# Optimization experiments

Measured on AMD Instinct MI355X. Metric: run time of the kernel, lower is better.

## Reference

```python
import jax, jax.numpy as jnp
import numpy as np

EMBED_DIM = 768
NUM_HEADS = 12
HEAD_DIM = EMBED_DIM // NUM_HEADS
SCALE = HEAD_DIM ** -0.5
LN_EPS = 1e-5


def layer_norm(x, gamma, beta):
    mu = jnp.mean(x, axis=-1, keepdims=True)
    var = jnp.var(x, axis=-1, keepdims=True)
    return (x - mu) * jax.lax.rsqrt(var + LN_EPS) * gamma + beta


def setup_inputs() -> dict:
    key = jax.random.key(0)
    ks = jax.random.split(key, 10)
    B, N, M, C = 4, 4096, 256, EMBED_DIM
    inp = {
        "input_tokens": jax.random.normal(ks[0], (B, N, C), dtype=jnp.float32),
        "query_tokens": jax.random.normal(ks[1], (B, M, C), dtype=jnp.float32),
        "Wq": jax.random.normal(ks[2], (C, C), dtype=jnp.float32) * 0.02,
        "bq": jnp.zeros((C,), dtype=jnp.float32),
        "Wk": jax.random.normal(ks[3], (C, C), dtype=jnp.float32) * 0.02,
        "bk": jnp.zeros((C,), dtype=jnp.float32),
        "Wv": jax.random.normal(ks[4], (C, C), dtype=jnp.float32) * 0.02,
        "bv": jnp.zeros((C,), dtype=jnp.float32),
        "gq_ln": jnp.ones((C,), dtype=jnp.float32),
        "bq_ln": jnp.zeros((C,), dtype=jnp.float32),
        "gk_ln": jnp.ones((C,), dtype=jnp.float32),
        "bk_ln": jnp.zeros((C,), dtype=jnp.float32),
    }
    return inp


def reference(input_tokens, query_tokens, Wq, bq, Wk, bk, Wv, bv,
              gq_ln, bq_ln, gk_ln, bk_ln):
    B, N, C = input_tokens.shape
    _, M, _ = query_tokens.shape
    H, D = NUM_HEADS, HEAD_DIM

    # v: Linear only (no LayerNorm on the attn=None path)
    v = (input_tokens @ Wv.T + bv).reshape(B, N, H, D).transpose(0, 2, 1, 3)   # [B,H,N,D]
    # q, k: Linear -> LayerNorm over full embed_dim, then split heads
    q = layer_norm(query_tokens @ Wq.T + bq, gq_ln, bq_ln)
    q = q.reshape(B, M, H, D).transpose(0, 2, 1, 3) * SCALE                    # [B,H,M,D]
    k = layer_norm(input_tokens @ Wk.T + bk, gk_ln, bk_ln)
    k = k.reshape(B, N, H, D).transpose(0, 2, 1, 3)                            # [B,H,N,D]

    attn = jax.nn.softmax(jnp.einsum('bhmd,bhnd->bhmn', q, k), axis=-1)        # [B,H,M,N]
    out = jnp.einsum('bhmn,bhnd->bhmd', attn, v)                               # [B,H,M,D]
    out = out.transpose(0, 2, 1, 3).reshape(B, M, C)
    return (query_tokens + out, attn)
```

## Files before the change

### kernel.cpp

```cpp
#include <hip/hip_runtime.h>
#include <math.h>

#define BB 4
#define NN 4096
#define MM 256
#define CC 768
#define HH 12
#define DD 64
#define SCALEF 0.125f
#define LN_EPSF 1e-5f

typedef __attribute__((ext_vector_type(4))) float f32x4;
typedef __attribute__((ext_vector_type(16))) float f32x16;
typedef __attribute__((ext_vector_type(8))) _Float16 f16x8;
typedef __attribute__((ext_vector_type(4))) _Float16 f16x4;

__device__ __forceinline__ void gldh(const _Float16* g, _Float16* l) {
    __builtin_amdgcn_global_load_lds(
        (const __attribute__((address_space(1))) void*)g,
        (__attribute__((address_space(3))) void*)l, 16, 0, 0);
}

__global__ __launch_bounds__(256) void conv_f16(
    const float* __restrict__ x, _Float16* __restrict__ y, long long n)
{
    long long i = ((long long)blockIdx.x * 256 + threadIdx.x) * 8;
    const long long stride = (long long)gridDim.x * 256 * 8;
    for (; i < n; i += stride) {
        float4 a = *(const float4*)(x + i);
        float4 b = *(const float4*)(x + i + 4);
        f16x8 o;
        o[0] = (_Float16)a.x; o[1] = (_Float16)a.y;
        o[2] = (_Float16)a.z; o[3] = (_Float16)a.w;
        o[4] = (_Float16)b.x; o[5] = (_Float16)b.y;
        o[6] = (_Float16)b.z; o[7] = (_Float16)b.w;
        *(f16x8*)(y + i) = o;
    }
}

__global__ __launch_bounds__(256) void proj_gemm_f16(
    const _Float16* __restrict__ Xh,
    const _Float16* __restrict__ X2h,
    const _Float16* __restrict__ Wkh, const _Float16* __restrict__ Wqh,
    const _Float16* __restrict__ Wvh,
    const float* __restrict__ bk, const float* __restrict__ bq,
    const float* __restrict__ bv,
    _Float16* __restrict__ Klin, _Float16* __restrict__ Qlin,
    _Float16* __restrict__ Vth)
{
    __shared__ _Float16 As[2][128 * 32];
    __shared__ _Float16 Bs[2][128 * 32];

    const int bid = blockIdx.x;
    const _Float16* Ag; const _Float16* Bg;
    const float* bias; _Float16* out = nullptr;
    int sid, bm, bn;
    bool isV = false;
    if (bid < 768) {
        sid = bid; Ag = Xh; Bg = Wkh; bias = bk; out = Klin;
        bm = sid & 127; bn = sid >> 7;
    } else if (bid < 816) {
        sid = bid - 768; Ag = X2h; Bg = Wqh; bias = bq; out = Qlin;
        bm = sid & 7; bn = sid >> 3;
    } else {
        sid = bid - 816; Ag = Xh; Bg = Wvh; bias = bv; isV = true;
        bm = sid & 127; bn = sid >> 7;
    }
    const int row0 = bm * 128, col0 = bn * 128;

    const int tid = threadIdx.x;
    const int w = tid >> 6, lane = tid & 63;
    const int wr = w >> 1, wc = w & 1;
    const int fr = lane & 15, kg = lane >> 4;

    f32x4 acc[4][4];
#pragma unroll
    for (int m = 0; m < 4; ++m)
#pragma unroll
        for (int n = 0; n < 4; ++n)
            acc[m][n] = (f32x4){0.f, 0.f, 0.f, 0.f};

#define STAGE(sel, kt)                                                          \
    do {                                                                        \
        const int kk = (kt) << 5;                                               \
        _Pragma("unroll")                                                       \
        for (int i = 0; i < 2; ++i) {                                           \
            const int cbase = (i * 4 + w) * 64;                                 \
            const int c = cbase + lane;                                         \
            const int row = c >> 2, ks = (c & 3) << 3;                          \
            gldh(Ag + (size_t)(row0 + row) * CC + kk + ks, &As[sel][cbase * 8]);\
            gldh(Bg + (size_t)(col0 + row) * CC + kk + ks, &Bs[sel][cbase * 8]);\
        }                                                                       \
    } while (0)

    STAGE(0, 0);
    int cur = 0;
    const int nk = CC >> 5;
    for (int kt = 0; kt < nk; ++kt) {
        __syncthreads();
        if (kt + 1 < nk) STAGE(cur ^ 1, kt + 1);
        const _Float16* lA = As[cur];
        const _Float16* lB = Bs[cur];
        f16x8 a[4], b[4];
#pragma unroll
        for (int m = 0; m < 4; ++m)
            a[m] = *(const f16x8*)(lA + (wr * 64 + m * 16 + fr) * 32 + kg * 8);
#pragma unroll
        for (int n = 0; n < 4; ++n)
            b[n] = *(const f16x8*)(lB + (wc * 64 + n * 16 + fr) * 32 + kg * 8);
        __builtin_amdgcn_s_setprio(1);
#pragma unroll
        for (int m = 0; m < 4; ++m)
#pragma unroll
            for (int n = 0; n < 4; ++n)
                acc[m][n] = __builtin_amdgcn_mfma_f32_16x16x32_f16(
                    a[m], b[n], acc[m][n], 0, 0, 0);
        __builtin_amdgcn_s_setprio(0);
        cur ^= 1;
    }
#undef STAGE

    if (!isV) {
        float bvv[4];
#pragma unroll
        for (int n = 0; n < 4; ++n)
            bvv[n] = bias[col0 + wc * 64 + n * 16 + fr];
#pragma unroll
        for (int m = 0; m < 4; ++m)
#pragma unroll
            for (int n = 0; n < 4; ++n) {
                const int col = col0 + wc * 64 + n * 16 + fr;
#pragma unroll
                for (int r = 0; r < 4; ++r) {
                    const int row = row0 + wr * 64 + m * 16 + kg * 4 + r;
                    out[(size_t)row * CC + col] = (_Float16)(acc[m][n][r] + bvv[n]);
                }
            }
    } else {
        const int b = row0 >> 12;
        const int rb = row0 & 4095;
#pragma unroll
        for (int n = 0; n < 4; ++n) {
            const int cg = col0 + wc * 64 + n * 16 + fr;
            const int hh = cg >> 6, d = cg & 63;
            const float bb = bias[cg];
            _Float16* vrow = Vth + ((size_t)((b * HH + hh) * DD + d)) * NN + rb + wr * 64;
#pragma unroll
            for (int m = 0; m < 4; ++m) {
                f16x4 v4;
#pragma unroll
                for (int r = 0; r < 4; ++r)
                    v4[r] = (_Float16)(acc[m][n][r] + bb);
                *(f16x4*)(vrow + m * 16 + kg * 4) = v4;
            }
        }
    }
}

__global__ __launch_bounds__(256) void ln_rows_f16(
    const _Float16* __restrict__ Y, _Float16* __restrict__ outh,
    const float* __restrict__ g, const float* __restrict__ be, const float scale)
{
    const int row = blockIdx.x;
    const _Float16* y = Y + (size_t)row * CC;
    const int tid = threadIdx.x;
    float x0 = (float)y[tid], x1 = (float)y[tid + 256], x2 = (float)y[tid + 512];
    float s = x0 + x1 + x2;
    float q = x0 * x0 + x1 * x1 + x2 * x2;
#pragma unroll
    for (int o = 32; o >= 1; o >>= 1) {
        s += __shfl_xor(s, o, 64);
        q += __shfl_xor(q, o, 64);
    }
    __shared__ float sh_s[4], sh_q[4];
    const int w = tid >> 6;
    if ((tid & 63) == 0) { sh_s[w] = s; sh_q[w] = q; }
    __syncthreads();
    s = sh_s[0] + sh_s[1] + sh_s[2] + sh_s[3];
    q = sh_q[0] + sh_q[1] + sh_q[2] + sh_q[3];
    const float mu  = s * (1.f / 768.f);
    const float var = q * (1.f / 768.f) - mu * mu;
    const float inv = rsqrtf(var + LN_EPSF);
    _Float16* o = outh + (size_t)row * CC;
    o[tid]       = (_Float16)(((x0 - mu) * inv * g[tid]       + be[tid])       * scale);
    o[tid + 256] = (_Float16)(((x1 - mu) * inv * g[tid + 256] + be[tid + 256]) * scale);
    o[tid + 512] = (_Float16)(((x2 - mu) * inv * g[tid + 512] + be[tid + 512]) * scale);
}

__global__ __launch_bounds__(256, 2) void fused_attn(
    const _Float16* __restrict__ Qh,
    const _Float16* __restrict__ Kh,
    const _Float16* __restrict__ Vt,
    const float* __restrict__ qtok,
    float* __restrict__ attn, float* __restrict__ out0)
{
    __shared__ __align__(16) unsigned char smem[78848];
    _Float16* Kl = (_Float16*)smem;
    _Float16* Vl = (_Float16*)(smem + 32768);
    _Float16* Ql = (_Float16*)(smem + 65536);
    _Float16* Pl = (_Float16*)(smem + 69632);
    float (*red)[32][2] = (float(*)[32][2])(smem + 77824);
    float* rbuf = (float*)smem;

    const int tid = threadIdx.x;
    const int w = tid >> 6, lane = tid & 63;
    const int l5 = lane >> 5, lm = lane & 31;
    const int bh = blockIdx.x % 48;
    const int mt = blockIdx.x / 48;
    const int h = bh % HH, b = bh / HH;
    const int qr0 = mt * 32;

#define STAGEK(sel, c0)                                                         \
    _Pragma("unroll")                                                           \
    for (int i = 0; i < 4; ++i) {                                               \
        const int L = i * 256 + tid;                                            \
        const int n = L >> 3, pos = L & 7;                                      \
        gldh(Kh + (size_t)(b * NN + (c0) + n) * CC + h * DD + ((pos ^ (n & 7)) << 3), \
             &Kl[(sel) * 8192 + (i * 256 + w * 64) * 8]);                       \
    }
#define STAGEV(sel, c0)                                                         \
    _Pragma("unroll")                                                           \
    for (int i = 0; i < 4; ++i) {                                               \
        const int L = i * 256 + tid;                                            \
        const int d = L >> 4, pos = L & 15;                                     \
        const int blk = (pos & 8) | ((pos & 7) ^ (d & 7));                      \
        gldh(Vt + (size_t)(bh * DD + d) * NN + (c0) + blk * 8,                  \
             &Vl[(sel) * 8192 + (i * 256 + w * 64) * 8]);                       \
    }

    {
        const int n = tid >> 3, pos = tid & 7;
        gldh(Qh + (size_t)(b * MM + qr0 + n) * CC + h * DD + ((pos ^ (n & 7)) << 3),
             &Ql[(w * 64) * 8]);
    }
    STAGEK(0, 0);
    __syncthreads();
    f16x8 qf[4];
#pragma unroll
    for (int ks = 0; ks < 4; ++ks)
        qf[ks] = *(const f16x8*)&Ql[lm * 64 + (((ks * 2 + l5) ^ (lm & 7)) << 3)];

    const int nl = w * 32 + lm;

    float mrun = -1e30f, srun = 0.f;
    int cur = 0;
    for (int c = 0; c < 32; ++c) {
        if (c) __syncthreads();
        if (c + 1 < 32) STAGEK(cur ^ 1, (c + 1) * 128);
        const _Float16* Kb = Kl + cur * 8192;
        f32x16 s;
#pragma unroll
        for (int r = 0; r < 16; ++r) s[r] = 0.f;
        __builtin_amdgcn_s_setprio(1);
#pragma unroll
        for (int ks = 0; ks < 4; ++ks) {
            f16x8 kf = *(const f16x8*)&Kb[nl * 64 + (((ks * 2 + l5) ^ (nl & 7)) << 3)];
            s = __builtin_amdgcn_mfma_f32_32x32x16_f16(kf, qf[ks], s, 0, 0, 0);
        }
        __builtin_amdgcn_s_setprio(0);
        float cmax = s[0];
#pragma unroll
        for (int r = 1; r < 16; ++r) cmax = fmaxf(cmax, s[r]);
        cmax = fmaxf(cmax, __shfl_xor(cmax, 32, 64));
        const float nm = fmaxf(mrun, cmax);
        float cs = 0.f;
#pragma unroll
        for (int r = 0; r < 16; ++r) cs += __expf(s[r] - nm);
        cs += __shfl_xor(cs, 32, 64);
        srun = srun * __expf(mrun - nm) + cs;
        mrun = nm;
        cur ^= 1;
    }
    if (lane < 32) { red[w][lane][0] = mrun; red[w][lane][1] = srun; }
    __syncthreads();
    float M = -1e30f;
#pragma unroll
    for (int ww = 0; ww < 4; ++ww) M = fmaxf(M, red[ww][lm][0]);
    float S = 0.f;
#pragma unroll
    for (int ww = 0; ww < 4; ++ww) S += red[ww][lm][1] * __expf(red[ww][lm][0] - M);
    const float invS = 1.f / S;

    f32x16 oacc[2];
#pragma unroll
    for (int dt = 0; dt < 2; ++dt)
#pragma unroll
        for (int r = 0; r < 16; ++r) oacc[dt][r] = 0.f;

    float* attnRow = attn + ((size_t)(bh * MM + qr0 + lm)) * NN;

    STAGEK(0, 0); STAGEV(0, 0);
    cur = 0;
    for (int c = 0; c < 32; ++c) {
        __syncthreads();
        if (c + 1 < 32) { STAGEK(cur ^ 1, (c + 1) * 128); STAGEV(cur ^ 1, (c + 1) * 128); }
        const _Float16* Kb = Kl + cur * 8192;
        const _Float16* Vb = Vl + cur * 8192;
        f32x16 s;
#pragma unroll
        for (int r = 0; r < 16; ++r) s[r] = 0.f;
        __builtin_amdgcn_s_setprio(1);
#pragma unroll
        for (int ks = 0; ks < 4; ++ks) {
            f16x8 kf = *(const f16x8*)&Kb[nl * 64 + (((ks * 2 + l5) ^ (nl & 7)) << 3)];
            s = __builtin_amdgcn_mfma_f32_32x32x16_f16(kf, qf[ks], s, 0, 0, 0);
        }
        __builtin_amdgcn_s_setprio(0);
#pragma unroll
        for (int q = 0; q < 4; ++q) {
            float4 pw;
            f16x4 ph;
#pragma unroll
            for (int r = 0; r < 4; ++r) {
                const float p = __expf(s[q * 4 + r] - M) * invS;
                ((float*)&pw)[r] = p;
                ph[r] = (_Float16)p;
            }
            *(float4*)(attnRow + c * 128 + w * 32 + q * 8 + l5 * 4) = pw;
            const int blk16 = w * 4 + q;
            const int pos = (blk16 & 8) | ((blk16 & 7) ^ (lm & 7));
            *(f16x4*)&Pl[lm * 128 + pos * 8 + l5 * 4] = ph;
        }
        __builtin_amdgcn_s_setprio(1);
#pragma unroll
        for (int ks = 0; ks < 2; ++ks) {
            const int blk16 = w * 4 + ks * 2 + l5;
            const int posP = (blk16 & 8) | ((blk16 & 7) ^ (lm & 7));
            f16x8 pf = *(const f16x8*)&Pl[lm * 128 + posP * 8];
#pragma unroll
            for (int dt = 0; dt < 2; ++dt) {
                const int d = dt * 32 + lm;
                const int posV = (blk16 & 8) | ((blk16 & 7) ^ (d & 7));
                f16x8 vf = *(const f16x8*)&Vb[d * 128 + posV * 8];
                oacc[dt] = __builtin_amdgcn_mfma_f32_32x32x16_f16(pf, vf, oacc[dt], 0, 0, 0);
            }
        }
        __builtin_amdgcn_s_setprio(0);
        cur ^= 1;
    }

    __syncthreads();
#pragma unroll
    for (int dt = 0; dt < 2; ++dt)
#pragma unroll
        for (int r = 0; r < 16; ++r) {
            const int mrow = (r & 3) + 8 * (r >> 2) + 4 * l5;
            rbuf[w * 2048 + mrow * 64 + dt * 32 + lm] = oacc[dt][r];
        }
    __syncthreads();
    {
        const int m = tid >> 3, d0 = (tid & 7) * 8;
        const size_t obase = (size_t)(b * MM + qr0 + m) * CC + h * DD + d0;
#pragma unroll
        for (int j = 0; j < 8; ++j) {
            const int idx = m * 64 + d0 + j;
            float v = rbuf[idx] + rbuf[2048 + idx] + rbuf[4096 + idx] + rbuf[6144 + idx];
            out0[obase + j] = v + qtok[obase + j];
        }
    }
#undef STAGEK
#undef STAGEV
}

extern "C" void kernel_launch(void* const* d_in, const int* in_sizes, int n_in,
                              void* d_out, int out_size, void* d_ws, size_t ws_size,
                              hipStream_t stream) {
    (void)in_sizes; (void)n_in; (void)out_size; (void)ws_size;
    const float* input_tokens = (const float*)d_in[0];
    const float* query_tokens = (const float*)d_in[1];
    const float* Wq   = (const float*)d_in[2];
    const float* bq   = (const float*)d_in[3];
    const float* Wk   = (const float*)d_in[4];
    const float* bk   = (const float*)d_in[5];
    const float* Wv   = (const float*)d_in[6];
    const float* bv   = (const float*)d_in[7];
    const float* gq   = (const float*)d_in[8];
    const float* bqln = (const float*)d_in[9];
    const float* gk   = (const float*)d_in[10];
    const float* bkln = (const float*)d_in[11];

    float* out0 = (float*)d_out;
    float* attn = out0 + (size_t)BB * MM * CC;

    _Float16* h   = (_Float16*)d_ws;
    _Float16* Klin = h;
    _Float16* Qlin = Klin + (size_t)BB * NN * CC;
    _Float16* Xh   = Qlin + (size_t)BB * MM * CC;
    _Float16* X2h  = Xh   + (size_t)BB * NN * CC;
    _Float16* Wkh  = X2h  + (size_t)BB * MM * CC;
    _Float16* Wqh  = Wkh  + (size_t)CC * CC;
    _Float16* Wvh  = Wqh  + (size_t)CC * CC;
    _Float16* Kh   = Wvh  + (size_t)CC * CC;
    _Float16* Qh   = Kh   + (size_t)BB * NN * CC;
    _Float16* Vt   = Qh   + (size_t)BB * MM * CC;

    conv_f16<<<2048, 256, 0, stream>>>(input_tokens, Xh, (long long)BB * NN * CC);
    conv_f16<<<384, 256, 0, stream>>>(query_tokens, X2h, (long long)BB * MM * CC);
    conv_f16<<<288, 256, 0, stream>>>(Wk, Wkh, (long long)CC * CC);
    conv_f16<<<288, 256, 0, stream>>>(Wq, Wqh, (long long)CC * CC);
    conv_f16<<<288, 256, 0, stream>>>(Wv, Wvh, (long long)CC * CC);

    proj_gemm_f16<<<1584, 256, 0, stream>>>(Xh, X2h, Wkh, Wqh, Wvh,
                                            bk, bq, bv, Klin, Qlin, Vt);

    ln_rows_f16<<<BB * NN, 256, 0, stream>>>(Klin, Kh, gk, bkln, 1.0f);
    ln_rows_f16<<<BB * MM, 256, 0, stream>>>(Qlin, Qh, gq, bqln, SCALEF);

    fused_attn<<<BB * HH * (MM / 32), 256, 0, stream>>>(Qh, Kh, Vt, query_tokens,
                                                        attn, out0);
}
```

Before: 215.4 us.

## Split attention over key dimension into stats, main and reduce kernels

The single fused attention kernel, which launched only 384 blocks, becomes three kernels that split the key sequence into four chunks for 1536 blocks. A stats kernel computes per-chunk row max and sum, the main kernel merges them, writes normalized attention probabilities and partial P·V outputs, and a reduce kernel sums the partials and adds the query residual. The aim is to fill the MI355X compute units, which were under-occupied. The cost is two extra launches and extra global traffic for the stats and partial buffers.

```diff
diff --git a/kernel.cpp b/kernel.cpp
--- a/kernel.cpp
+++ b/kernel.cpp
@@ -187,28 +187,117 @@
     o[tid + 512] = (_Float16)(((x2 - mu) * inv * g[tid + 512] + be[tid + 512]) * scale);
 }
 
-__global__ __launch_bounds__(256, 2) void fused_attn(
+__global__ __launch_bounds__(256, 4) void attn_stats(
     const _Float16* __restrict__ Qh,
     const _Float16* __restrict__ Kh,
+    float* __restrict__ stats)
+{
+    __shared__ __align__(16) unsigned char smem[37888];
+    _Float16* Kl = (_Float16*)smem;
+    _Float16* Ql = (_Float16*)(smem + 32768);
+    float (*red)[32][2] = (float(*)[32][2])(smem + 36864);
+
+    const int tid = threadIdx.x;
+    const int w = tid >> 6, lane = tid & 63;
+    const int l5 = lane >> 5, lm = lane & 31;
+    const int bid = blockIdx.x;
+    const int mt = bid / 192;
+    const int rem = bid % 192;
+    const int bh = rem >> 2, ns = rem & 3;
+    const int h = bh % HH, b = bh / HH;
+    const int qr0 = mt * 32;
+    const int nb = ns * 1024;
+
+#define STAGEK(sel, c0)                                                         \
+    _Pragma("unroll")                                                           \
+    for (int i = 0; i < 4; ++i) {                                               \
+        const int L = i * 256 + tid;                                            \
+        const int n = L >> 3, pos = L & 7;                                      \
+        gldh(Kh + (size_t)(b * NN + (c0) + n) * CC + h * DD + ((pos ^ (n & 7)) << 3), \
+             &Kl[(sel) * 8192 + (i * 256 + w * 64) * 8]);                       \
+    }
+
+    {
+        const int n = tid >> 3, pos = tid & 7;
+        gldh(Qh + (size_t)(b * MM + qr0 + n) * CC + h * DD + ((pos ^ (n & 7)) << 3),
+             &Ql[(w * 64) * 8]);
+    }
+    STAGEK(0, nb);
+    __syncthreads();
+    f16x8 qf[4];
+#pragma unroll
+    for (int ks = 0; ks < 4; ++ks)
+        qf[ks] = *(const f16x8*)&Ql[lm * 64 + (((ks * 2 + l5) ^ (lm & 7)) << 3)];
+
+    const int nl = w * 32 + lm;
+
+    float mrun = -1e30f, srun = 0.f;
+    int cur = 0;
+    for (int c = 0; c < 8; ++c) {
+        if (c) __syncthreads();
+        if (c + 1 < 8) STAGEK(cur ^ 1, nb + (c + 1) * 128);
+        const _Float16* Kb = Kl + cur * 8192;
+        f32x16 s;
+#pragma unroll
+        for (int r = 0; r < 16; ++r) s[r] = 0.f;
+        __builtin_amdgcn_s_setprio(1);
+#pragma unroll
+        for (int ks = 0; ks < 4; ++ks) {
+            f16x8 kf = *(const f16x8*)&Kb[nl * 64 + (((ks * 2 + l5) ^ (nl & 7)) << 3)];
+            s = __builtin_amdgcn_mfma_f32_32x32x16_f16(kf, qf[ks], s, 0, 0, 0);
+        }
+        __builtin_amdgcn_s_setprio(0);
+        float cmax = s[0];
+#pragma unroll
+        for (int r = 1; r < 16; ++r) cmax = fmaxf(cmax, s[r]);
+        cmax = fmaxf(cmax, __shfl_xor(cmax, 32, 64));
+        const float nm = fmaxf(mrun, cmax);
+        float cs = 0.f;
+#pragma unroll
+        for (int r = 0; r < 16; ++r) cs += __expf(s[r] - nm);
+        cs += __shfl_xor(cs, 32, 64);
+        srun = srun * __expf(mrun - nm) + cs;
+        mrun = nm;
+        cur ^= 1;
+    }
+    if (lane < 32) { red[w][lane][0] = mrun; red[w][lane][1] = srun; }
+    __syncthreads();
+    if (w == 0 && lane < 32) {
+        float M = -1e30f;
+#pragma unroll
+        for (int ww = 0; ww < 4; ++ww) M = fmaxf(M, red[ww][lane][0]);
+        float S = 0.f;
+#pragma unroll
+        for (int ww = 0; ww < 4; ++ww) S += red[ww][lane][1] * __expf(red[ww][lane][0] - M);
+        float* sp = stats + ((size_t)((bh * 8 + mt) * 32 + lane)) * 8 + ns * 2;
+        sp[0] = M; sp[1] = S;
+    }
+#undef STAGEK
+}
+
+__global__ __launch_bounds__(256, 2) void attn_main(
+    const _Float16* __restrict__ Qh, const _Float16* __restrict__ Kh,
     const _Float16* __restrict__ Vt,
-    const float* __restrict__ qtok,
-    float* __restrict__ attn, float* __restrict__ out0)
+    const float* __restrict__ stats,
+    float* __restrict__ attn, float* __restrict__ part)
 {
-    __shared__ __align__(16) unsigned char smem[78848];
+    __shared__ __align__(16) unsigned char smem[77824];
     _Float16* Kl = (_Float16*)smem;
     _Float16* Vl = (_Float16*)(smem + 32768);
     _Float16* Ql = (_Float16*)(smem + 65536);
     _Float16* Pl = (_Float16*)(smem + 69632);
-    float (*red)[32][2] = (float(*)[32][2])(smem + 77824);
     float* rbuf = (float*)smem;
 
     const int tid = threadIdx.x;
     const int w = tid >> 6, lane = tid & 63;
     const int l5 = lane >> 5, lm = lane & 31;
-    const int bh = blockIdx.x % 48;
-    const int mt = blockIdx.x / 48;
+    const int bid = blockIdx.x;
+    const int mt = bid / 192;
+    const int rem = bid % 192;
+    const int bh = rem >> 2, ns = rem & 3;
     const int h = bh % HH, b = bh / HH;
     const int qr0 = mt * 32;
+    const int nb = ns * 1024;
 
 #define STAGEK(sel, c0)                                                         \
     _Pragma("unroll")                                                           \
@@ -228,12 +317,24 @@
              &Vl[(sel) * 8192 + (i * 256 + w * 64) * 8]);                       \
     }
 
+    float M, invS;
+    {
+        const float* sp = stats + ((size_t)((bh * 8 + mt) * 32 + lm)) * 8;
+        M = -1e30f;
+#pragma unroll
+        for (int n2 = 0; n2 < 4; ++n2) M = fmaxf(M, sp[n2 * 2]);
+        float S = 0.f;
+#pragma unroll
+        for (int n2 = 0; n2 < 4; ++n2) S += sp[n2 * 2 + 1] * __expf(sp[n2 * 2] - M);
+        invS = 1.f / S;
+    }
+
     {
         const int n = tid >> 3, pos = tid & 7;
         gldh(Qh + (size_t)(b * MM + qr0 + n) * CC + h * DD + ((pos ^ (n & 7)) << 3),
              &Ql[(w * 64) * 8]);
     }
-    STAGEK(0, 0);
+    STAGEK(0, nb); STAGEV(0, nb);
     __syncthreads();
     f16x8 qf[4];
 #pragma unroll
@@ -242,58 +343,18 @@
 
     const int nl = w * 32 + lm;
 
-    float mrun = -1e30f, srun = 0.f;
+    f32x16 oacc[2];
+#pragma unroll
+    for (int dt = 0; dt < 2; ++dt)
+#pragma unroll
+        for (int r = 0; r < 16; ++r) oacc[dt][r] = 0.f;
+
+    float* attnRow = attn + ((size_t)(bh * MM + qr0 + lm)) * NN + nb;
+
     int cur = 0;
-    for (int c = 0; c < 32; ++c) {
+    for (int c = 0; c < 8; ++c) {
         if (c) __syncthreads();
-        if (c + 1 < 32) STAGEK(cur ^ 1, (c + 1) * 128);
-        const _Float16* Kb = Kl + cur * 8192;
-        f32x16 s;
-#pragma unroll
-        for (int r = 0; r < 16; ++r) s[r] = 0.f;
-        __builtin_amdgcn_s_setprio(1);
-#pragma unroll
-        for (int ks = 0; ks < 4; ++ks) {
-            f16x8 kf = *(const f16x8*)&Kb[nl * 64 + (((ks * 2 + l5) ^ (nl & 7)) << 3)];
-            s = __builtin_amdgcn_mfma_f32_32x32x16_f16(kf, qf[ks], s, 0, 0, 0);
-        }
-        __builtin_amdgcn_s_setprio(0);
-        float cmax = s[0];
-#pragma unroll
-        for (int r = 1; r < 16; ++r) cmax = fmaxf(cmax, s[r]);
-        cmax = fmaxf(cmax, __shfl_xor(cmax, 32, 64));
-        const float nm = fmaxf(mrun, cmax);
-        float cs = 0.f;
-#pragma unroll
-        for (int r = 0; r < 16; ++r) cs += __expf(s[r] - nm);
-        cs += __shfl_xor(cs, 32, 64);
-        srun = srun * __expf(mrun - nm) + cs;
-        mrun = nm;
-        cur ^= 1;
-    }
-    if (lane < 32) { red[w][lane][0] = mrun; red[w][lane][1] = srun; }
-    __syncthreads();
-    float M = -1e30f;
-#pragma unroll
-    for (int ww = 0; ww < 4; ++ww) M = fmaxf(M, red[ww][lm][0]);
-    float S = 0.f;
-#pragma unroll
-    for (int ww = 0; ww < 4; ++ww) S += red[ww][lm][1] * __expf(red[ww][lm][0] - M);
-    const float invS = 1.f / S;
-
-    f32x16 oacc[2];
-#pragma unroll
-    for (int dt = 0; dt < 2; ++dt)
-#pragma unroll
-        for (int r = 0; r < 16; ++r) oacc[dt][r] = 0.f;
-
-    float* attnRow = attn + ((size_t)(bh * MM + qr0 + lm)) * NN;
-
-    STAGEK(0, 0); STAGEV(0, 0);
-    cur = 0;
-    for (int c = 0; c < 32; ++c) {
-        __syncthreads();
-        if (c + 1 < 32) { STAGEK(cur ^ 1, (c + 1) * 128); STAGEV(cur ^ 1, (c + 1) * 128); }
+        if (c + 1 < 8) { STAGEK(cur ^ 1, nb + (c + 1) * 128); STAGEV(cur ^ 1, nb + (c + 1) * 128); }
         const _Float16* Kb = Kl + cur * 8192;
         const _Float16* Vb = Vl + cur * 8192;
         f32x16 s;
@@ -350,16 +411,52 @@
     __syncthreads();
     {
         const int m = tid >> 3, d0 = (tid & 7) * 8;
-        const size_t obase = (size_t)(b * MM + qr0 + m) * CC + h * DD + d0;
-#pragma unroll
-        for (int j = 0; j < 8; ++j) {
+        const int rglob = bh * MM + qr0 + m;
+        float* pp = part + ((size_t)ns * (BB * HH * MM) + rglob) * DD + d0;
+        float4 v0, v1;
+#pragma unroll
+        for (int j = 0; j < 4; ++j) {
             const int idx = m * 64 + d0 + j;
-            float v = rbuf[idx] + rbuf[2048 + idx] + rbuf[4096 + idx] + rbuf[6144 + idx];
-            out0[obase + j] = v + qtok[obase + j];
-        }
+            ((float*)&v0)[j] = rbuf[idx] + rbuf[2048 + idx] + rbuf[4096 + idx] + rbuf[6144 + idx];
+        }
+#pragma unroll
+        for (int j = 0; j < 4; ++j) {
+            const int idx = m * 64 + d0 + 4 + j;
+            ((float*)&v1)[j] = rbuf[idx] + rbuf[2048 + idx] + rbuf[4096 + idx] + rbuf[6144 + idx];
+        }
+        *(float4*)(pp) = v0;
+        *(float4*)(pp + 4) = v1;
     }
 #undef STAGEK
 #undef STAGEV
+}
+
+__global__ __launch_bounds__(256) void attn_reduce(
+    const float* __restrict__ part, const float* __restrict__ qtok,
+    float* __restrict__ out0)
+{
+    const int g = blockIdx.x * 256 + threadIdx.x;
+    const int row = g >> 3, d0 = (g & 7) * 8;
+    const int bh = row >> 8, m = row & 255;
+    const int b = bh / HH, h = bh % HH;
+    const size_t pbase = (size_t)row * DD + d0;
+    const size_t R = (size_t)(BB * HH * MM) * DD;
+    float4 a0 = *(const float4*)(part + pbase);
+    float4 a1 = *(const float4*)(part + pbase + 4);
+#pragma unroll
+    for (int ns = 1; ns < 4; ++ns) {
+        float4 b0 = *(const float4*)(part + ns * R + pbase);
+        float4 b1 = *(const float4*)(part + ns * R + pbase + 4);
+        a0.x += b0.x; a0.y += b0.y; a0.z += b0.z; a0.w += b0.w;
+        a1.x += b1.x; a1.y += b1.y; a1.z += b1.z; a1.w += b1.w;
+    }
+    const size_t o = ((size_t)(b * MM + m)) * CC + h * DD + d0;
+    float4 q0 = *(const float4*)(qtok + o);
+    float4 q1 = *(const float4*)(qtok + o + 4);
+    a0.x += q0.x; a0.y += q0.y; a0.z += q0.z; a0.w += q0.w;
+    a1.x += q1.x; a1.y += q1.y; a1.z += q1.z; a1.w += q1.w;
+    *(float4*)(out0 + o) = a0;
+    *(float4*)(out0 + o + 4) = a1;
 }
 
 extern "C" void kernel_launch(void* const* d_in, const int* in_sizes, int n_in,
@@ -382,8 +479,8 @@
     float* out0 = (float*)d_out;
     float* attn = out0 + (size_t)BB * MM * CC;
 
-    _Float16* h   = (_Float16*)d_ws;
-    _Float16* Klin = h;
+    _Float16* hptr = (_Float16*)d_ws;
+    _Float16* Klin = hptr;
     _Float16* Qlin = Klin + (size_t)BB * NN * CC;
     _Float16* Xh   = Qlin + (size_t)BB * MM * CC;
     _Float16* X2h  = Xh   + (size_t)BB * NN * CC;
@@ -393,6 +490,8 @@
     _Float16* Kh   = Wvh  + (size_t)CC * CC;
     _Float16* Qh   = Kh   + (size_t)BB * NN * CC;
     _Float16* Vt   = Qh   + (size_t)BB * MM * CC;
+    float* stats   = (float*)(Vt + (size_t)BB * HH * DD * NN);
+    float* part    = stats + (size_t)BB * HH * MM * 8;
 
     conv_f16<<<2048, 256, 0, stream>>>(input_tokens, Xh, (long long)BB * NN * CC);
     conv_f16<<<384, 256, 0, stream>>>(query_tokens, X2h, (long long)BB * MM * CC);
@@ -406,6 +505,7 @@
     ln_rows_f16<<<BB * NN, 256, 0, stream>>>(Klin, Kh, gk, bkln, 1.0f);
     ln_rows_f16<<<BB * MM, 256, 0, stream>>>(Qlin, Qh, gq, bqln, SCALEF);
 
-    fused_attn<<<BB * HH * (MM / 32), 256, 0, stream>>>(Qh, Kh, Vt, query_tokens,
-                                                        attn, out0);
-}
+    attn_stats<<<1536, 256, 0, stream>>>(Qh, Kh, stats);
+    attn_main<<<1536, 256, 0, stream>>>(Qh, Kh, Vt, stats, attn, part);
+    attn_reduce<<<384, 256, 0, stream>>>(part, query_tokens, out0);
+}
```

Result: slower. 240.5 us (+11.6%).
